# Performance work log

Measured on AMD Instinct MI355X. Metric: run time of the kernel, lower is better.

Reference implementation:

```python
import jax, jax.numpy as jnp
import numpy as np

B, N, K, D = 8, 4096, 16, 256


def layer_norm(x, g, b, eps=1e-5):
    m = jnp.mean(x, axis=-1, keepdims=True)
    v = jnp.var(x, axis=-1, keepdims=True)
    return (x - m) * jax.lax.rsqrt(v + eps) * g + b


def setup_inputs() -> dict:
    key = jax.random.key(0)
    ks = jax.random.split(key, 8)

    def lin(k, fi, fo):
        return (jax.random.normal(k, (fi, fo), jnp.float32) / np.sqrt(fi).astype(np.float32),
                jnp.zeros((fo,), jnp.float32))

    coordinates = jax.random.normal(ks[0], (B, N, 3), jnp.float32)
    W1, b1 = lin(ks[1], 10, D // 4)
    W2, b2 = lin(ks[2], D // 4, D // 2)
    W3, b3 = lin(ks[3], D // 2, D)
    Wa1, ba1 = lin(ks[4], D, D)
    Wa2, ba2 = lin(ks[5], D, D)
    return {
        'coordinates': coordinates,
        'W1': W1, 'b1': b1, 'g1': jnp.ones((D // 4,)), 'be1': jnp.zeros((D // 4,)),
        'W2': W2, 'b2': b2, 'g2': jnp.ones((D // 2,)), 'be2': jnp.zeros((D // 2,)),
        'W3': W3, 'b3': b3, 'g3': jnp.ones((D,)), 'be3': jnp.zeros((D,)),
        'Wa1': Wa1, 'ba1': ba1, 'ga1': jnp.ones((D,)), 'bea1': jnp.zeros((D,)),
        'Wa2': Wa2, 'ba2': ba2,
    }


def reference(coordinates, W1, b1, g1, be1, W2, b2, g2, be2, W3, b3, g3, be3,
              Wa1, ba1, ga1, bea1, Wa2, ba2):
    # kNN via squared-distance matrix (monotone in Euclidean distance)
    sq = jnp.sum(coordinates * coordinates, axis=-1)  # [B,N]
    d2 = sq[:, :, None] + sq[:, None, :] - 2.0 * jnp.einsum('bnd,bmd->bnm', coordinates, coordinates)
    _, idx = jax.lax.top_k(-d2, K)  # smallest K distances, [B,N,K]

    nbr = jax.vmap(lambda c, i: c[i])(coordinates, idx)  # [B,N,K,3]
    rel = nbr - coordinates[:, :, None, :]               # relative positions
    dist = jnp.linalg.norm(rel, axis=-1, keepdims=True)  # [B,N,K,1]
    rn = rel / (dist + 1e-6)
    axy = jnp.arctan2(rn[..., 1], rn[..., 0])[..., None]
    axz = jnp.arctan2(rn[..., 2], rn[..., 0])[..., None]
    ayz = jnp.arctan2(rn[..., 2], rn[..., 1])[..., None]
    geom = jnp.concatenate([dist, rel, axy, axz, ayz, rn], axis=-1)  # [B,N,K,10]

    # encoder MLP
    h = jax.nn.relu(layer_norm(geom @ W1 + b1, g1, be1))
    h = jax.nn.relu(layer_norm(h @ W2 + b2, g2, be2))
    h = layer_norm(h @ W3 + b3, g3, be3)

    agg = jnp.mean(h, axis=2)  # mean over neighbors -> [B,N,D]

    # aggregator MLP
    out = jax.nn.relu(layer_norm(agg @ Wa1 + ba1, ga1, bea1)) @ Wa2 + ba2
    return out
```

## Files before the change

kernel.cpp:

```cpp
#include <hip/hip_runtime.h>
#include <hip/hip_bf16.h>
#include <math.h>

#define BB 8
#define NN 4096
#define KK 16
#define DD 256

typedef __hip_bfloat16 bf16;
typedef _Float16 half8 __attribute__((ext_vector_type(8)));
typedef float f32x4 __attribute__((ext_vector_type(4)));

union HFU { _Float16 h; unsigned short u; };
__device__ __forceinline__ unsigned short f2h(float x) { HFU v; v.h = (_Float16)x; return v.u; }

#define CONV_TOTAL 273344
#define O_COORD 0
#define O_W1 98304
#define O_b1 98944
#define O_g1 99008
#define O_be1 99072
#define O_W2 99136
#define O_b2 107328
#define O_g2 107456
#define O_be2 107584
#define O_W3 107712
#define O_b3 140480
#define O_g3 140736
#define O_be3 140992
#define O_Wa1 141248
#define O_ba1 206784
#define O_ga1 207040
#define O_bea1 207296
#define O_Wa2 207552
#define O_ba2 273088

#define F_W1 0
#define F_W2 2048
#define F_W3 10240
#define F_A1 43008
#define F_A2 108544
#define FRAG_TOTAL 174080

struct SrcPtrs {
  const void* p[19];
};

__global__ __launch_bounds__(256) void convert_kernel(SrcPtrs sp, float* __restrict__ dst) {
  static constexpr int OFF[20] = {
      0,      98304,  98944,  99008,  99072,  99136,  107328, 107456, 107584,
      107712, 140480, 140736, 140992, 141248, 206784, 207040, 207296, 207552,
      273088, 273344};
  const int i = blockIdx.x * 256 + threadIdx.x;
  if (i >= CONV_TOTAL) return;
  const unsigned tag = ((const unsigned*)sp.p[3])[0];
  const bool isb = (tag == 0x3F803F80u);
  int s = 0;
#pragma unroll
  for (int j = 1; j < 19; j++)
    if (i >= OFF[j]) s = j;
  const int local = i - OFF[s];
  float v = isb ? __bfloat162float(((const bf16*)sp.p[s])[local])
                : ((const float*)sp.p[s])[local];
  dst[i] = v;
}

__global__ __launch_bounds__(256) void swizzle_kernel(const float* __restrict__ conv,
                                                      unsigned short* __restrict__ frag) {
  const int t = blockIdx.x * 256 + threadIdx.x;
  if (t >= FRAG_TOTAL) return;
  int l, e;
  if (t < 2048) { l = 0; e = t; }
  else if (t < 10240) { l = 1; e = t - 2048; }
  else if (t < 43008) { l = 2; e = t - 10240; }
  else if (t < 108544) { l = 3; e = t - 43008; }
  else { l = 4; e = t - 108544; }
  static constexpr int WOFF[5] = {O_W1, O_W2, O_W3, O_Wa1, O_Wa2};
  static constexpr int NDIM[5] = {64, 128, 256, 256, 256};
  static constexpr int NTC[5] = {4, 8, 16, 16, 16};
  static constexpr int KREAL[5] = {10, 64, 128, 256, 256};
  static constexpr int HOFF[5] = {F_W1, F_W2, F_W3, F_A1, F_A2};
  const int j = e & 7;
  const int lane = (e >> 3) & 63;
  const int tile = e >> 9;
  const int nt = tile % NTC[l];
  const int kt = tile / NTC[l];
  const int k = kt * 32 + (lane >> 4) * 8 + j;
  const int n = nt * 16 + (lane & 15);
  float w = (k < KREAL[l]) ? conv[WOFF[l] + k * NDIM[l] + n] : 0.0f;
  frag[HOFF[l] + e] = f2h(w);
}

__device__ __forceinline__ float sq3_rn(float x, float y, float z) {
  return __fadd_rn(__fadd_rn(__fmul_rn(x, x), __fmul_rn(y, y)), __fmul_rn(z, z));
}
__device__ __forceinline__ float dot3_rn(float ax, float ay, float az, float bx, float by, float bz) {
  return __fadd_rn(__fadd_rn(__fmul_rn(ax, bx), __fmul_rn(ay, by)), __fmul_rn(az, bz));
}
__device__ __forceinline__ unsigned f2ord(float f) {
  unsigned u = __float_as_uint(f);
  return (u & 0x80000000u) ? ~u : (u | 0x80000000u);
}
__device__ __forceinline__ float ord2f(unsigned o) {
  unsigned u = (o & 0x80000000u) ? (o & 0x7FFFFFFFu) : ~o;
  return __uint_as_float(u);
}

__device__ __forceinline__ unsigned long long bitonic64(unsigned long long key, int lane) {
#pragma unroll
  for (int k = 2; k <= 64; k <<= 1) {
#pragma unroll
    for (int jj = k >> 1; jj > 0; jj >>= 1) {
      unsigned long long v = __shfl_xor(key, jj, 64);
      bool asc = ((lane & k) == 0);
      bool up = ((lane & jj) != 0);
      unsigned long long mn = (key < v) ? key : v;
      unsigned long long mx2 = (key < v) ? v : key;
      key = (up == asc) ? mx2 : mn;
    }
  }
  return key;
}

__global__ __launch_bounds__(512) void cellsort_kernel(const float* __restrict__ conv,
                                                       float4* __restrict__ sorted,
                                                       int* __restrict__ sidx) {
  __shared__ unsigned hist[512];
  __shared__ unsigned scanb[512];
  const int b = blockIdx.x;
  const int tid = threadIdx.x;
  const float* cb = conv + O_COORD + (size_t)b * NN * 3;
  hist[tid] = 0;
  __syncthreads();
  float xs[8], ys[8], zs[8];
  int cell[8];
  unsigned rank[8];
#pragma unroll
  for (int u = 0; u < 8; u++) {
    int p = u * 512 + tid;
    float x = cb[p * 3 + 0], y = cb[p * 3 + 1], z = cb[p * 3 + 2];
    xs[u] = x; ys[u] = y; zs[u] = z;
    int ix = min(7, max(0, (int)floorf(x + 4.0f)));
    int iy = min(7, max(0, (int)floorf(y + 4.0f)));
    int iz = min(7, max(0, (int)floorf(z + 4.0f)));
    int m = ((ix & 1) | ((ix & 2) << 2) | ((ix & 4) << 4)) |
            (((iy & 1) | ((iy & 2) << 2) | ((iy & 4) << 4)) << 1) |
            (((iz & 1) | ((iz & 2) << 2) | ((iz & 4) << 4)) << 2);
    cell[u] = m;
    rank[u] = atomicAdd(&hist[m], 1u);
  }
  __syncthreads();
  scanb[tid] = hist[tid];
  __syncthreads();
  for (int off = 1; off < 512; off <<= 1) {
    unsigned t = (tid >= off) ? scanb[tid - off] : 0u;
    __syncthreads();
    scanb[tid] += t;
    __syncthreads();
  }
#pragma unroll
  for (int u = 0; u < 8; u++) {
    unsigned base = scanb[cell[u]] - hist[cell[u]];
    unsigned pos = base + rank[u];
    sorted[(size_t)b * NN + pos] =
        make_float4(xs[u], ys[u], zs[u], sq3_rn(xs[u], ys[u], zs[u]));
    sidx[(size_t)b * NN + pos] = u * 512 + tid;
  }
}

__global__ __launch_bounds__(64) void knn_wave_kernel(const float4* __restrict__ soa,
                                                      const int* __restrict__ sI,
                                                      int* __restrict__ idx_out) {
  const int lane = threadIdx.x;
  const int wid = blockIdx.x;
  const int q0 = wid * 4;
  const int b = q0 >> 12;
  const float4* P = soa + (size_t)b * NN;
  const int* I = sI + (size_t)b * NN;
  const int qr = q0 & (NN - 1);
  const int base = qr >> 6;

  float cx[4], cy[4], cz[4], sqn[4];
  int qix[4];
#pragma unroll
  for (int j = 0; j < 4; j++) {
    float4 c = P[qr + j];
    cx[j] = c.x; cy[j] = c.y; cz[j] = c.z; sqn[j] = c.w;
    qix[j] = I[qr + j];
  }

  unsigned long long R[4], pend[4];
  float tauf[4];
  int A[4] = {0, 0, 0, 0};
#pragma unroll
  for (int j = 0; j < 4; j++) pend[j] = ~0ull;

  auto MERGE = [&](int j) {
    unsigned long long key =
        (lane < 16) ? R[j] : ((lane < 16 + A[j]) ? pend[j] : ~0ull);
    key = bitonic64(key, lane);
    R[j] = key;
    tauf[j] = ord2f((unsigned)(unsigned long long)__builtin_amdgcn_readlane(
        (int)(unsigned)(key >> 32), 15));
    A[j] = 0;
  };

  auto APPEND = [&](int j, unsigned long long msk, int cc, unsigned long long key) {
    unsigned rank = __builtin_amdgcn_mbcnt_hi(
        (unsigned)(msk >> 32), __builtin_amdgcn_mbcnt_lo((unsigned)msk, 0u));
    const bool flag = ((msk >> lane) & 1ull) != 0;
    const int lim = 16 + A[j];
    const int nf = lane - (int)rank;
    const int dst = flag ? (lim + (int)rank) : (nf < lim ? nf : nf + cc);
    int src = __builtin_amdgcn_ds_permute(dst << 2, lane) & 63;
    unsigned lo = (unsigned)__builtin_amdgcn_ds_bpermute(src << 2, (int)(unsigned)key);
    unsigned hi = (unsigned)__builtin_amdgcn_ds_bpermute(src << 2, (int)(unsigned)(key >> 32));
    const bool cons = (lane >= lim) && (lane < lim + cc);
    if (cons) pend[j] = (((unsigned long long)hi) << 32) | lo;
    A[j] += cc;
  };

  const int b0 = base * 64 + lane;
  float4 f0 = P[b0];
  int i0 = I[b0];
  const int b1 = ((base + 1) & 63) * 64 + lane;
  float4 f1 = P[b1];
  int i1 = I[b1];
  const int b2i = ((base + 2) & 63) * 64 + lane;
  float4 f2 = P[b2i];
  int i2 = I[b2i];

#pragma unroll
  for (int j = 0; j < 4; j++) {
    float dot = dot3_rn(cx[j], cy[j], cz[j], f0.x, f0.y, f0.z);
    float d2 = __fsub_rn(__fadd_rn(sqn[j], f0.w), __fmul_rn(2.0f, dot));
    unsigned long long key =
        (((unsigned long long)f2ord(d2)) << 32) | (unsigned)i0;
    key = bitonic64(key, lane);
    R[j] = key;
    tauf[j] = ord2f((unsigned)(unsigned long long)__builtin_amdgcn_readlane(
        (int)(unsigned)(key >> 32), 15));
  }

  for (int t = 1; t < 64; t++) {
    const float4 c = f1;
    const int iv = i1;
    f1 = f2; i1 = i2;
    if (t + 2 < 64) {
      const int nb = ((base + t + 2) & 63) * 64 + lane;
      f2 = P[nb];
      i2 = I[nb];
    }
    float d2v[4];
    unsigned long long pm[4];
#pragma unroll
    for (int j = 0; j < 4; j++) {
      float dot = dot3_rn(cx[j], cy[j], cz[j], c.x, c.y, c.z);
      d2v[j] = __fsub_rn(__fadd_rn(sqn[j], c.w), __fmul_rn(2.0f, dot));
      pm[j] = __ballot(d2v[j] <= tauf[j]);
    }
    if (!(pm[0] | pm[1] | pm[2] | pm[3])) continue;
#pragma unroll
    for (int j = 0; j < 4; j++) {
      unsigned long long rem = pm[j];
      if (!rem) continue;
      const unsigned long long key =
          (((unsigned long long)f2ord(d2v[j])) << 32) | (unsigned)iv;
      int cc = __builtin_popcountll(rem);
      while (A[j] + cc > 48) {
        if (A[j] == 0) {
          unsigned long long take = rem & 0xFFFFFFFFull;
          APPEND(j, take, __builtin_popcountll(take), key);
          rem ^= take;
        }
        MERGE(j);
        rem &= __ballot(d2v[j] <= tauf[j]);
        cc = __builtin_popcountll(rem);
      }
      if (cc) APPEND(j, rem, cc, key);
    }
  }

#pragma unroll
  for (int j = 0; j < 4; j++) {
    if (A[j]) MERGE(j);
    if (lane < KK)
      idx_out[((size_t)b * NN + (unsigned)qix[j]) * KK + lane] =
          (int)(R[j] & 0xFFFFFFFFull);
  }
}

template <int KT>
__device__ __forceinline__ void load_afrags(half8* A, const unsigned short* lF,
                                            int rowe, int lane) {
#pragma unroll
  for (int kt = 0; kt < KT; kt++) {
    int off = (lane & 15) * rowe + kt * 32 + (lane >> 4) * 8;
    A[kt] = *reinterpret_cast<const half8*>(lF + off);
  }
}

template <int NT>
__device__ __forceinline__ void init_acc(f32x4* acc, const float* __restrict__ bias,
                                         int lane) {
  const int col = lane & 15;
#pragma unroll
  for (int nt = 0; nt < NT; nt++) {
    float bv = bias[nt * 16 + col];
    acc[nt] = {bv, bv, bv, bv};
  }
}

template <int KT, int NT>
__device__ __forceinline__ void gemm_acc(f32x4* acc, const half8* A,
                                         const unsigned short* bb, int lane) {
#pragma unroll
  for (int kt = 0; kt < KT; kt++)
#pragma unroll
    for (int nt = 0; nt < NT; nt++) {
      const half8 bf = *reinterpret_cast<const half8*>(bb + (kt * NT + nt) * 512 + lane * 8);
      acc[nt] = __builtin_amdgcn_mfma_f32_16x16x32_f16(A[kt], bf, acc[nt], 0, 0, 0);
    }
}

template <int NT>
__device__ __forceinline__ void ln_stats(const f32x4* acc, float* m, float* rs) {
  float s[4] = {0.f, 0.f, 0.f, 0.f}, s2[4] = {0.f, 0.f, 0.f, 0.f};
#pragma unroll
  for (int nt = 0; nt < NT; nt++)
#pragma unroll
    for (int r = 0; r < 4; r++) {
      float v = acc[nt][r];
      s[r] += v;
      s2[r] += v * v;
    }
#pragma unroll
  for (int msk = 1; msk <= 8; msk <<= 1)
#pragma unroll
    for (int r = 0; r < 4; r++) {
      s[r] += __shfl_xor(s[r], msk, 64);
      s2[r] += __shfl_xor(s2[r], msk, 64);
    }
  const float invN = 1.0f / (NT * 16);
#pragma unroll
  for (int r = 0; r < 4; r++) {
    m[r] = s[r] * invN;
    float var = s2[r] * invN - m[r] * m[r];
    rs[r] = rsqrtf(var + 1e-5f);
  }
}

template <int NT, bool RELU>
__device__ __forceinline__ void ln_store(const f32x4* acc, const float* m, const float* rs,
                                         const float* __restrict__ g, const float* __restrict__ be,
                                         unsigned short* lF, int rowe, int lane) {
  const int col = lane & 15;
  const int rbase = (lane >> 4) * 4;
#pragma unroll
  for (int nt = 0; nt < NT; nt++) {
    float gv = g[nt * 16 + col], bv = be[nt * 16 + col];
#pragma unroll
    for (int r = 0; r < 4; r++) {
      float v = (acc[nt][r] - m[r]) * rs[r] * gv + bv;
      if (RELU) v = fmaxf(v, 0.0f);
      lF[(rbase + r) * rowe + nt * 16 + col] = f2h(v);
    }
  }
}

__device__ __forceinline__ void stage_b(unsigned short* bbuf,
                                        const unsigned short* __restrict__ src,
                                        int n_u4, int tid) {
  const uint4* s = reinterpret_cast<const uint4*>(src);
  uint4* d = reinterpret_cast<uint4*>(bbuf);
  for (int i = tid; i < n_u4; i += 256) d[i] = s[i];
}

#define ROWE_E 136
#define PSTR_E (16 * ROWE_E)

__global__ __launch_bounds__(256, 4) void encoder_mfma(
    const float* __restrict__ conv, const int* __restrict__ nbr,
    const unsigned short* __restrict__ frag, unsigned short* __restrict__ agF) {
  __shared__ unsigned short planes[4 * PSTR_E];
  __shared__ unsigned short Bbuf[10240];
  const int tid = threadIdx.x;
  const int lane = tid & 63;
  const int wave = tid >> 6;
  const int point = blockIdx.x * 4 + wave;
  const int b = point >> 12;
  const int n = point & (NN - 1);
  const float* cb = conv + O_COORD + (size_t)b * NN * 3;
  unsigned short* lF = planes + wave * PSTR_E;
  const int g = lane >> 4;
  const int col = lane & 15;

  {
    int pl = tid >> 6, row = (tid >> 2) & 15, part = tid & 3;
    *reinterpret_cast<uint4*>(planes + pl * PSTR_E + row * ROWE_E + part * 8) =
        make_uint4(0u, 0u, 0u, 0u);
    stage_b(Bbuf, frag + F_W1, 1280, tid);
  }
  __syncthreads();

  {
    const int nb = col;
    const int part = g;
    float cxq = cb[n * 3 + 0], cyq = cb[n * 3 + 1], czq = cb[n * 3 + 2];
    int id = nbr[(size_t)point * KK + nb];
    float rx = __fsub_rn(cb[id * 3 + 0], cxq);
    float ry = __fsub_rn(cb[id * 3 + 1], cyq);
    float rz = __fsub_rn(cb[id * 3 + 2], czq);
    float dist = __fsqrt_rn(sq3_rn(rx, ry, rz));
    float den = __fadd_rn(dist, 1e-6f);
    float ux = __fdiv_rn(rx, den), uy = __fdiv_rn(ry, den), uz = __fdiv_rn(rz, den);
    float ya = (part == 0) ? uy : uz;
    float xa = (part == 2) ? uy : ux;
    float ang = atan2f(ya, xa);
    if (part < 3) {
      lF[nb * ROWE_E + 4 + part] = f2h(ang);
    } else {
      unsigned short* r0 = lF + nb * ROWE_E;
      r0[0] = f2h(dist); r0[1] = f2h(rx); r0[2] = f2h(ry); r0[3] = f2h(rz);
      r0[7] = f2h(ux); r0[8] = f2h(uy); r0[9] = f2h(uz);
    }
  }

  {
    half8 x0;
    load_afrags<1>(&x0, lF, ROWE_E, lane);
    f32x4 a1[4];
#pragma unroll
    for (int m = 0; m < 4; m++) {
      const float4 bv = *reinterpret_cast<const float4*>(conv + O_b1 + m * 16 + g * 4);
      a1[m] = {bv.x, bv.y, bv.z, bv.w};
      const half8 wf = *reinterpret_cast<const half8*>(Bbuf + m * 512 + lane * 8);
      a1[m] = __builtin_amdgcn_mfma_f32_16x16x32_f16(wf, x0, a1[m], 0, 0, 0);
    }
    float s = 0.f, s2 = 0.f;
#pragma unroll
    for (int m = 0; m < 4; m++)
#pragma unroll
      for (int r = 0; r < 4; r++) { float v = a1[m][r]; s += v; s2 += v * v; }
    s += __shfl_xor(s, 16, 64); s += __shfl_xor(s, 32, 64);
    s2 += __shfl_xor(s2, 16, 64); s2 += __shfl_xor(s2, 32, 64);
    const float mu = s * (1.0f / 64.0f);
    const float rsg = rsqrtf(s2 * (1.0f / 64.0f) - mu * mu + 1e-5f);
#pragma unroll
    for (int m = 0; m < 4; m++) {
      const float4 gv = *reinterpret_cast<const float4*>(conv + O_g1 + m * 16 + g * 4);
      const float4 bev = *reinterpret_cast<const float4*>(conv + O_be1 + m * 16 + g * 4);
      float v0 = fmaxf((a1[m][0] - mu) * rsg * gv.x + bev.x, 0.0f);
      float v1 = fmaxf((a1[m][1] - mu) * rsg * gv.y + bev.y, 0.0f);
      float v2 = fmaxf((a1[m][2] - mu) * rsg * gv.z + bev.z, 0.0f);
      float v3 = fmaxf((a1[m][3] - mu) * rsg * gv.w + bev.w, 0.0f);
      uint2 pk;
      pk.x = (unsigned)f2h(v0) | ((unsigned)f2h(v1) << 16);
      pk.y = (unsigned)f2h(v2) | ((unsigned)f2h(v3) << 16);
      *reinterpret_cast<uint2*>(lF + col * ROWE_E + m * 16 + g * 4) = pk;
    }
  }

  {
    half8 x2[2];
    load_afrags<2>(x2, lF, ROWE_E, lane);
    f32x4 a2[8];
#pragma unroll
    for (int m = 0; m < 8; m++) {
      const float4 bv = *reinterpret_cast<const float4*>(conv + O_b2 + m * 16 + g * 4);
      a2[m] = {bv.x, bv.y, bv.z, bv.w};
    }
#pragma unroll
    for (int kt = 0; kt < 2; kt++)
#pragma unroll
      for (int m = 0; m < 8; m++) {
        const half8 wf =
            *reinterpret_cast<const half8*>(Bbuf + 2048 + (kt * 8 + m) * 512 + lane * 8);
        a2[m] = __builtin_amdgcn_mfma_f32_16x16x32_f16(wf, x2[kt], a2[m], 0, 0, 0);
      }
    float s = 0.f, s2 = 0.f;
#pragma unroll
    for (int m = 0; m < 8; m++)
#pragma unroll
      for (int r = 0; r < 4; r++) { float v = a2[m][r]; s += v; s2 += v * v; }
    s += __shfl_xor(s, 16, 64); s += __shfl_xor(s, 32, 64);
    s2 += __shfl_xor(s2, 16, 64); s2 += __shfl_xor(s2, 32, 64);
    const float mu = s * (1.0f / 128.0f);
    const float rsg = rsqrtf(s2 * (1.0f / 128.0f) - mu * mu + 1e-5f);
#pragma unroll
    for (int m = 0; m < 8; m++) {
      const float4 gv = *reinterpret_cast<const float4*>(conv + O_g2 + m * 16 + g * 4);
      const float4 bev = *reinterpret_cast<const float4*>(conv + O_be2 + m * 16 + g * 4);
      float v0 = fmaxf((a2[m][0] - mu) * rsg * gv.x + bev.x, 0.0f);
      float v1 = fmaxf((a2[m][1] - mu) * rsg * gv.y + bev.y, 0.0f);
      float v2 = fmaxf((a2[m][2] - mu) * rsg * gv.z + bev.z, 0.0f);
      float v3 = fmaxf((a2[m][3] - mu) * rsg * gv.w + bev.w, 0.0f);
      uint2 pk;
      pk.x = (unsigned)f2h(v0) | ((unsigned)f2h(v1) << 16);
      pk.y = (unsigned)f2h(v2) | ((unsigned)f2h(v3) << 16);
      *reinterpret_cast<uint2*>(lF + col * ROWE_E + m * 16 + g * 4) = pk;
    }
  }

  half8 A3[4];
  load_afrags<4>(A3, lF, ROWE_E, lane);
  f32x4 acc[16];
  init_acc<16>(acc, conv + O_b3, lane);
  {
    const unsigned short* W3 = frag + F_W3;
#pragma unroll
    for (int kt = 0; kt < 4; kt++)
#pragma unroll
      for (int nt = 0; nt < 16; nt++) {
        const half8 bf =
            *reinterpret_cast<const half8*>(W3 + (kt * 16 + nt) * 512 + lane * 8);
        acc[nt] = __builtin_amdgcn_mfma_f32_16x16x32_f16(A3[kt], bf, acc[nt], 0, 0, 0);
      }
  }

  {
    float m[4], rs[4];
    ln_stats<16>(acc, m, rs);
    float sv[16];
#pragma unroll
    for (int nt = 0; nt < 16; nt++) {
      float gvv = conv[O_g3 + nt * 16 + col], bvv = conv[O_be3 + nt * 16 + col];
      float s = 0.f;
#pragma unroll
      for (int r = 0; r < 4; r++) s += (acc[nt][r] - m[r]) * rs[r] * gvv + bvv;
      s += __shfl_xor(s, 16, 64);
      s += __shfl_xor(s, 32, 64);
      sv[nt] = s * (1.0f / 16.0f);
    }
    if (lane < 16) {
      size_t base = (size_t)point * DD;
#pragma unroll
      for (int nt = 0; nt < 16; nt++) agF[base + nt * 16 + lane] = f2h(sv[nt]);
    }
  }
}

#define ROWE_A 264

__global__ __launch_bounds__(256) void aggmlp_mfma(
    const float* __restrict__ conv, const unsigned short* __restrict__ agF,
    const unsigned short* __restrict__ a1, const unsigned short* __restrict__ a2,
    const unsigned* __restrict__ g1raw, void* __restrict__ out) {
  __shared__ unsigned short lds[4][16 * ROWE_A];
  const int lane = threadIdx.x & 63;
  const int wave = threadIdx.x >> 6;
  const int row0 = (blockIdx.x * 4 + wave) * 16;
  unsigned short* lF = lds[wave];

#pragma unroll
  for (int t = 0; t < 8; t++) {
    int v = t * 64 + lane;
    int row = v >> 5;
    int c0 = (v & 31) * 8;
    *reinterpret_cast<uint4*>(lF + row * ROWE_A + c0) =
        *reinterpret_cast<const uint4*>(agF + ((size_t)(row0 + row) * DD + c0));
  }
  __syncthreads();

  float m[4], rs[4];
  f32x4 acc[16];
  {
    half8 A[8];
    load_afrags<8>(A, lF, ROWE_A, lane);
    init_acc<16>(acc, conv + O_ba1, lane);
    gemm_acc<8, 16>(acc, A, a1, lane);
    ln_stats<16>(acc, m, rs);
    ln_store<16, true>(acc, m, rs, conv + O_ga1, conv + O_bea1, lF, ROWE_A, lane);
  }
  __syncthreads();
  {
    half8 A[8];
    load_afrags<8>(A, lF, ROWE_A, lane);
    init_acc<16>(acc, conv + O_ba2, lane);
    gemm_acc<8, 16>(acc, A, a2, lane);
  }
  const bool isb = (g1raw[0] == 0x3F803F80u);
  const int col = lane & 15;
  const int rbase = (lane >> 4) * 4;
  if (isb) {
    bf16* o = (bf16*)out;
#pragma unroll
    for (int nt = 0; nt < 16; nt++)
#pragma unroll
      for (int r = 0; r < 4; r++)
        o[(size_t)(row0 + rbase + r) * DD + nt * 16 + col] = __float2bfloat16(acc[nt][r]);
  } else {
    float* o = (float*)out;
#pragma unroll
    for (int nt = 0; nt < 16; nt++)
#pragma unroll
      for (int r = 0; r < 4; r++)
        o[(size_t)(row0 + rbase + r) * DD + nt * 16 + col] = acc[nt][r];
  }
}

extern "C" void kernel_launch(void* const* d_in, const int* in_sizes, int n_in,
                              void* d_out, int out_size, void* d_ws, size_t ws_size,
                              hipStream_t stream) {
  char* ws = (char*)d_ws;
  float* conv = (float*)ws;
  int* idx_ws = (int*)(ws + 1093376);
  unsigned short* agF = (unsigned short*)(ws + 3190528);
  unsigned short* frag = (unsigned short*)(ws + 19967744);
  float4* sorted = (float4*)(ws + 20315904);
  int* sidx = (int*)(ws + 20840192);

  SrcPtrs sp;
  for (int i = 0; i < 19; i++) sp.p[i] = d_in[i];

  convert_kernel<<<(CONV_TOTAL + 255) / 256, 256, 0, stream>>>(sp, conv);
  swizzle_kernel<<<(FRAG_TOTAL + 255) / 256, 256, 0, stream>>>(conv, frag);
  cellsort_kernel<<<BB, 512, 0, stream>>>(conv, sorted, sidx);

  knn_wave_kernel<<<BB * NN / 4, 64, 0, stream>>>(sorted, sidx, idx_ws);

  encoder_mfma<<<BB * NN / 4, 256, 0, stream>>>(conv, idx_ws, frag, agF);

  aggmlp_mfma<<<BB * NN / 64, 256, 0, stream>>>(conv, agF, frag + F_A1, frag + F_A2,
                                                (const unsigned*)d_in[3], d_out);
}
```

Measured before the change: 389.8 us.

## Transpose MFMA operands in MLPs, drop LDS weight staging, simplify LN-mean epilogue

The encoder no longer stages W1/W2 fragments into shared memory and drops the block-wide barrier, reading the weight fragments directly from global memory. The final LayerNorm-then-mean-over-neighbours step is rewritten algebraically so the mean and gamma/beta are applied once per column instead of per element. The aggregator MLP swaps MFMA operands (weights as A, activations as B), so each lane holds four contiguous output columns. That layout allows vectorised float4/uint2 stores and packed fp16 LDS writes, and the now-unneeded __syncthreads are removed. The trade-off is more global/L2 weight traffic in the encoder in exchange for less LDS use and fewer synchronisations.

```diff
diff --git a/kernel.cpp b/kernel.cpp
--- a/kernel.cpp
+++ b/kernel.cpp
@@ -13,6 +13,8 @@
 
 union HFU { _Float16 h; unsigned short u; };
 __device__ __forceinline__ unsigned short f2h(float x) { HFU v; v.h = (_Float16)x; return v.u; }
+union BFU { bf16 b; unsigned short u; };
+__device__ __forceinline__ unsigned short f2b(float x) { BFU v; v.b = __float2bfloat16(x); return v.u; }
 
 #define CONV_TOTAL 273344
 #define O_COORD 0
@@ -311,18 +313,6 @@
   }
 }
 
-template <int KT, int NT>
-__device__ __forceinline__ void gemm_acc(f32x4* acc, const half8* A,
-                                         const unsigned short* bb, int lane) {
-#pragma unroll
-  for (int kt = 0; kt < KT; kt++)
-#pragma unroll
-    for (int nt = 0; nt < NT; nt++) {
-      const half8 bf = *reinterpret_cast<const half8*>(bb + (kt * NT + nt) * 512 + lane * 8);
-      acc[nt] = __builtin_amdgcn_mfma_f32_16x16x32_f16(A[kt], bf, acc[nt], 0, 0, 0);
-    }
-}
-
 template <int NT>
 __device__ __forceinline__ void ln_stats(const f32x4* acc, float* m, float* rs) {
   float s[4] = {0.f, 0.f, 0.f, 0.f}, s2[4] = {0.f, 0.f, 0.f, 0.f};
@@ -350,32 +340,6 @@
   }
 }
 
-template <int NT, bool RELU>
-__device__ __forceinline__ void ln_store(const f32x4* acc, const float* m, const float* rs,
-                                         const float* __restrict__ g, const float* __restrict__ be,
-                                         unsigned short* lF, int rowe, int lane) {
-  const int col = lane & 15;
-  const int rbase = (lane >> 4) * 4;
-#pragma unroll
-  for (int nt = 0; nt < NT; nt++) {
-    float gv = g[nt * 16 + col], bv = be[nt * 16 + col];
-#pragma unroll
-    for (int r = 0; r < 4; r++) {
-      float v = (acc[nt][r] - m[r]) * rs[r] * gv + bv;
-      if (RELU) v = fmaxf(v, 0.0f);
-      lF[(rbase + r) * rowe + nt * 16 + col] = f2h(v);
-    }
-  }
-}
-
-__device__ __forceinline__ void stage_b(unsigned short* bbuf,
-                                        const unsigned short* __restrict__ src,
-                                        int n_u4, int tid) {
-  const uint4* s = reinterpret_cast<const uint4*>(src);
-  uint4* d = reinterpret_cast<uint4*>(bbuf);
-  for (int i = tid; i < n_u4; i += 256) d[i] = s[i];
-}
-
 #define ROWE_E 136
 #define PSTR_E (16 * ROWE_E)
 
@@ -383,7 +347,6 @@
     const float* __restrict__ conv, const int* __restrict__ nbr,
     const unsigned short* __restrict__ frag, unsigned short* __restrict__ agF) {
   __shared__ unsigned short planes[4 * PSTR_E];
-  __shared__ unsigned short Bbuf[10240];
   const int tid = threadIdx.x;
   const int lane = tid & 63;
   const int wave = tid >> 6;
@@ -396,12 +359,10 @@
   const int col = lane & 15;
 
   {
-    int pl = tid >> 6, row = (tid >> 2) & 15, part = tid & 3;
-    *reinterpret_cast<uint4*>(planes + pl * PSTR_E + row * ROWE_E + part * 8) =
+    int row = (tid >> 2) & 15, part = tid & 3;
+    *reinterpret_cast<uint4*>(lF + row * ROWE_E + part * 8) =
         make_uint4(0u, 0u, 0u, 0u);
-    stage_b(Bbuf, frag + F_W1, 1280, tid);
-  }
-  __syncthreads();
+  }
 
   {
     const int nb = col;
@@ -434,7 +395,7 @@
     for (int m = 0; m < 4; m++) {
       const float4 bv = *reinterpret_cast<const float4*>(conv + O_b1 + m * 16 + g * 4);
       a1[m] = {bv.x, bv.y, bv.z, bv.w};
-      const half8 wf = *reinterpret_cast<const half8*>(Bbuf + m * 512 + lane * 8);
+      const half8 wf = *reinterpret_cast<const half8*>(frag + F_W1 + m * 512 + lane * 8);
       a1[m] = __builtin_amdgcn_mfma_f32_16x16x32_f16(wf, x0, a1[m], 0, 0, 0);
     }
     float s = 0.f, s2 = 0.f;
@@ -474,8 +435,8 @@
     for (int kt = 0; kt < 2; kt++)
 #pragma unroll
       for (int m = 0; m < 8; m++) {
-        const half8 wf =
-            *reinterpret_cast<const half8*>(Bbuf + 2048 + (kt * 8 + m) * 512 + lane * 8);
+        const half8 wf = *reinterpret_cast<const half8*>(
+            frag + F_W2 + (kt * 8 + m) * 512 + lane * 8);
         a2[m] = __builtin_amdgcn_mfma_f32_16x16x32_f16(wf, x2[kt], a2[m], 0, 0, 0);
       }
     float s = 0.f, s2 = 0.f;
@@ -521,16 +482,20 @@
   {
     float m[4], rs[4];
     ln_stats<16>(acc, m, rs);
+    float rs16[4];
+#pragma unroll
+    for (int r = 0; r < 4; r++) rs16[r] = rs[r] * 0.0625f;
+    float S = m[0] * rs16[0] + m[1] * rs16[1] + m[2] * rs16[2] + m[3] * rs16[3];
+    S += __shfl_xor(S, 16, 64);
+    S += __shfl_xor(S, 32, 64);
     float sv[16];
 #pragma unroll
     for (int nt = 0; nt < 16; nt++) {
-      float gvv = conv[O_g3 + nt * 16 + col], bvv = conv[O_be3 + nt * 16 + col];
-      float s = 0.f;
-#pragma unroll
-      for (int r = 0; r < 4; r++) s += (acc[nt][r] - m[r]) * rs[r] * gvv + bvv;
-      s += __shfl_xor(s, 16, 64);
-      s += __shfl_xor(s, 32, 64);
-      sv[nt] = s * (1.0f / 16.0f);
+      float p = acc[nt][0] * rs16[0] + acc[nt][1] * rs16[1] +
+                acc[nt][2] * rs16[2] + acc[nt][3] * rs16[3];
+      p += __shfl_xor(p, 16, 64);
+      p += __shfl_xor(p, 32, 64);
+      sv[nt] = (p - S) * conv[O_g3 + nt * 16 + col] + conv[O_be3 + nt * 16 + col];
     }
     if (lane < 16) {
       size_t base = (size_t)point * DD;
@@ -551,6 +516,8 @@
   const int wave = threadIdx.x >> 6;
   const int row0 = (blockIdx.x * 4 + wave) * 16;
   unsigned short* lF = lds[wave];
+  const int g = lane >> 4;
+  const int col = lane & 15;
 
 #pragma unroll
   for (int t = 0; t < 8; t++) {
@@ -560,42 +527,84 @@
     *reinterpret_cast<uint4*>(lF + row * ROWE_A + c0) =
         *reinterpret_cast<const uint4*>(agF + ((size_t)(row0 + row) * DD + c0));
   }
-  __syncthreads();
-
-  float m[4], rs[4];
+
   f32x4 acc[16];
   {
-    half8 A[8];
-    load_afrags<8>(A, lF, ROWE_A, lane);
-    init_acc<16>(acc, conv + O_ba1, lane);
-    gemm_acc<8, 16>(acc, A, a1, lane);
-    ln_stats<16>(acc, m, rs);
-    ln_store<16, true>(acc, m, rs, conv + O_ga1, conv + O_bea1, lF, ROWE_A, lane);
-  }
-  __syncthreads();
-  {
-    half8 A[8];
-    load_afrags<8>(A, lF, ROWE_A, lane);
-    init_acc<16>(acc, conv + O_ba2, lane);
-    gemm_acc<8, 16>(acc, A, a2, lane);
-  }
+    half8 xb[8];
+    load_afrags<8>(xb, lF, ROWE_A, lane);
+#pragma unroll
+    for (int mt = 0; mt < 16; mt++) {
+      const float4 bv = *reinterpret_cast<const float4*>(conv + O_ba1 + mt * 16 + g * 4);
+      acc[mt] = {bv.x, bv.y, bv.z, bv.w};
+    }
+#pragma unroll
+    for (int kt = 0; kt < 8; kt++)
+#pragma unroll
+      for (int mt = 0; mt < 16; mt++) {
+        const half8 wf =
+            *reinterpret_cast<const half8*>(a1 + (kt * 16 + mt) * 512 + lane * 8);
+        acc[mt] = __builtin_amdgcn_mfma_f32_16x16x32_f16(wf, xb[kt], acc[mt], 0, 0, 0);
+      }
+    float s = 0.f, s2 = 0.f;
+#pragma unroll
+    for (int mt = 0; mt < 16; mt++)
+#pragma unroll
+      for (int r = 0; r < 4; r++) { float v = acc[mt][r]; s += v; s2 += v * v; }
+    s += __shfl_xor(s, 16, 64); s += __shfl_xor(s, 32, 64);
+    s2 += __shfl_xor(s2, 16, 64); s2 += __shfl_xor(s2, 32, 64);
+    const float mu = s * (1.0f / 256.0f);
+    const float rsg = rsqrtf(s2 * (1.0f / 256.0f) - mu * mu + 1e-5f);
+#pragma unroll
+    for (int mt = 0; mt < 16; mt++) {
+      const float4 gv = *reinterpret_cast<const float4*>(conv + O_ga1 + mt * 16 + g * 4);
+      const float4 bev = *reinterpret_cast<const float4*>(conv + O_bea1 + mt * 16 + g * 4);
+      float v0 = fmaxf((acc[mt][0] - mu) * rsg * gv.x + bev.x, 0.0f);
+      float v1 = fmaxf((acc[mt][1] - mu) * rsg * gv.y + bev.y, 0.0f);
+      float v2 = fmaxf((acc[mt][2] - mu) * rsg * gv.z + bev.z, 0.0f);
+      float v3 = fmaxf((acc[mt][3] - mu) * rsg * gv.w + bev.w, 0.0f);
+      uint2 pk;
+      pk.x = (unsigned)f2h(v0) | ((unsigned)f2h(v1) << 16);
+      pk.y = (unsigned)f2h(v2) | ((unsigned)f2h(v3) << 16);
+      *reinterpret_cast<uint2*>(lF + col * ROWE_A + mt * 16 + g * 4) = pk;
+    }
+  }
+
+  {
+    half8 xb[8];
+    load_afrags<8>(xb, lF, ROWE_A, lane);
+#pragma unroll
+    for (int mt = 0; mt < 16; mt++) {
+      const float4 bv = *reinterpret_cast<const float4*>(conv + O_ba2 + mt * 16 + g * 4);
+      acc[mt] = {bv.x, bv.y, bv.z, bv.w};
+    }
+#pragma unroll
+    for (int kt = 0; kt < 8; kt++)
+#pragma unroll
+      for (int mt = 0; mt < 16; mt++) {
+        const half8 wf =
+            *reinterpret_cast<const half8*>(a2 + (kt * 16 + mt) * 512 + lane * 8);
+        acc[mt] = __builtin_amdgcn_mfma_f32_16x16x32_f16(wf, xb[kt], acc[mt], 0, 0, 0);
+      }
+  }
+
   const bool isb = (g1raw[0] == 0x3F803F80u);
-  const int col = lane & 15;
-  const int rbase = (lane >> 4) * 4;
+  const size_t rbase = (size_t)(row0 + col) * DD;
   if (isb) {
     bf16* o = (bf16*)out;
 #pragma unroll
-    for (int nt = 0; nt < 16; nt++)
-#pragma unroll
-      for (int r = 0; r < 4; r++)
-        o[(size_t)(row0 + rbase + r) * DD + nt * 16 + col] = __float2bfloat16(acc[nt][r]);
+    for (int mt = 0; mt < 16; mt++) {
+      uint2 pk;
+      pk.x = (unsigned)f2b(acc[mt][0]) | ((unsigned)f2b(acc[mt][1]) << 16);
+      pk.y = (unsigned)f2b(acc[mt][2]) | ((unsigned)f2b(acc[mt][3]) << 16);
+      *reinterpret_cast<uint2*>(o + rbase + mt * 16 + g * 4) = pk;
+    }
   } else {
     float* o = (float*)out;
 #pragma unroll
-    for (int nt = 0; nt < 16; nt++)
-#pragma unroll
-      for (int r = 0; r < 4; r++)
-        o[(size_t)(row0 + rbase + r) * DD + nt * 16 + col] = acc[nt][r];
+    for (int mt = 0; mt < 16; mt++) {
+      float4 f = make_float4(acc[mt][0], acc[mt][1], acc[mt][2], acc[mt][3]);
+      *reinterpret_cast<float4*>(o + rbase + mt * 16 + g * 4) = f;
+    }
   }
 }
 
```

After: 444.2 us. 1.14x slower.
